# Performance work log

Hardware: AMD Instinct MI355X
Metric: run time of the kernel (lower is better)

The kernel has to match this reference:

```python
import jax, jax.numpy as jnp
import numpy as np

B, S, H, D = 4, 2048, 12, 64

def setup_inputs() -> dict:
    key = jax.random.key(0)
    kq, kk, kv_, kb = jax.random.split(key, 4)
    q = jax.random.normal(kq, (B, S, H, D), dtype=jnp.float32)
    k = jax.random.normal(kk, (B, S, H, D), dtype=jnp.float32)
    v = jax.random.normal(kv_, (B, S, H, D), dtype=jnp.float32)
    attn_bias = jax.random.normal(kb, (B, H, S, S), dtype=jnp.float32)
    return {"q": q, "k": k, "v": v, "attn_bias": attn_bias}

def reference(q, k, v, attn_bias):
    # flash_attn_func(q, k, v, attn_bias=bias): non-causal SDPA with additive bias,
    # softmax_scale = 1/sqrt(head_dim). Layout [b, s, h, d]; bias [b, h, sq, sk].
    scale = 1.0 / jnp.sqrt(jnp.asarray(q.shape[-1], q.dtype))
    # scores: [b, h, sq, sk]
    scores = jnp.einsum('bqhd,bkhd->bhqk', q, k) * scale + attn_bias
    probs = jax.nn.softmax(scores, axis=-1)
    out = jnp.einsum('bhqk,bkhd->bqhd', probs, v)
    return out
```

## Files before the change

kernel.cpp:

```cpp
#include <hip/hip_runtime.h>
#include <hip/hip_bf16.h>

#define B_ 4
#define S_ 2048
#define H_ 12
#define D_ 64
#define QT 64
#define KT 64
#define NQT (S_/QT)
#define NKT (S_/KT)
#define LOG2E 1.44269504088896340736f

typedef __bf16 bf16x8 __attribute__((ext_vector_type(8)));
typedef __bf16 bf16x4 __attribute__((ext_vector_type(4)));
typedef float  f32x4  __attribute__((ext_vector_type(4)));

__global__ __launch_bounds__(256, 2) void fa_fwd(
    const float* __restrict__ Q, const float* __restrict__ K,
    const float* __restrict__ V, const float* __restrict__ Bias,
    float* __restrict__ Out)
{
  __shared__ __attribute__((aligned(16))) __bf16 Qs[QT*72];
  __shared__ __attribute__((aligned(16))) __bf16 Ks[KT*72];
  __shared__ __attribute__((aligned(16))) __bf16 Vt[D_*68];
  __shared__ __attribute__((aligned(16))) __bf16 Ps[4*16*72];

  const int bid = blockIdx.x;
  const int qt  = bid & (NQT-1);
  const int bh  = bid >> 5;
  const int b   = bh / H_;
  const int h   = bh - b*H_;
  const int q0  = qt*QT;

  const int tid  = threadIdx.x;
  const int w    = tid >> 6;
  const int lane = tid & 63;
  const int g    = lane >> 4;
  const int c    = lane & 15;

  const float qscale = 0.125f * LOG2E;

  #pragma unroll
  for (int i = 0; i < 4; ++i) {
    int flat = i*256 + tid;
    int qr = flat >> 4;
    int d4 = (flat & 15) << 2;
    float4 qv = *(const float4*)(Q + (((size_t)b*S_ + q0 + qr)*H_ + h)*D_ + d4);
    bf16x4 pk;
    pk[0] = (__bf16)(qv.x * qscale); pk[1] = (__bf16)(qv.y * qscale);
    pk[2] = (__bf16)(qv.z * qscale); pk[3] = (__bf16)(qv.w * qscale);
    *(bf16x4*)&Qs[qr*72 + d4] = pk;
  }

  f32x4 Ov[4] = {};
  float m_i[4], l_i[4];
  #pragma unroll
  for (int r = 0; r < 4; ++r) { m_i[r] = -1e30f; l_i[r] = 0.f; }

  const size_t row_base = (size_t)q0 + 16*w + 4*g;
  const float* bb    = Bias + ((size_t)bh*S_ + row_base)*S_ + c;
  const float* kbase = K + ((size_t)b*S_*H_ + h)*D_;
  const float* vbase = V + ((size_t)b*S_*H_ + h)*D_;

  for (int kt = 0; kt < NKT; ++kt) {
    const int k0 = kt*KT;

    float bl[4][4];
    #pragma unroll
    for (int t = 0; t < 4; ++t)
      #pragma unroll
      for (int r = 0; r < 4; ++r)
        bl[t][r] = bb[(size_t)r*S_ + k0 + 16*t];

    __syncthreads();

    #pragma unroll
    for (int i = 0; i < 4; ++i) {
      int flat = i*256 + tid;
      int kr = flat >> 4;
      int d4 = (flat & 15) << 2;
      float4 kv = *(const float4*)(kbase + (size_t)(k0+kr)*H_*D_ + d4);
      bf16x4 pk;
      pk[0]=(__bf16)kv.x; pk[1]=(__bf16)kv.y; pk[2]=(__bf16)kv.z; pk[3]=(__bf16)kv.w;
      *(bf16x4*)&Ks[kr*72 + d4] = pk;
    }
    #pragma unroll
    for (int i = 0; i < 4; ++i) {
      int flat = i*256 + tid;
      int vr = flat >> 4;
      int d4 = (flat & 15) << 2;
      float4 vv = *(const float4*)(vbase + (size_t)(k0+vr)*H_*D_ + d4);
      Vt[(d4+0)*68 + vr] = (__bf16)vv.x;
      Vt[(d4+1)*68 + vr] = (__bf16)vv.y;
      Vt[(d4+2)*68 + vr] = (__bf16)vv.z;
      Vt[(d4+3)*68 + vr] = (__bf16)vv.w;
    }
    __syncthreads();

    bf16x8 aq0 = *(const bf16x8*)&Qs[(16*w + c)*72 + 8*g];
    bf16x8 aq1 = *(const bf16x8*)&Qs[(16*w + c)*72 + 32 + 8*g];
    float sc[4][4];
    #pragma unroll
    for (int t = 0; t < 4; ++t) {
      bf16x8 bk0 = *(const bf16x8*)&Ks[(16*t + c)*72 + 8*g];
      bf16x8 bk1 = *(const bf16x8*)&Ks[(16*t + c)*72 + 32 + 8*g];
      f32x4 acc = {};
      acc = __builtin_amdgcn_mfma_f32_16x16x32_bf16(aq0, bk0, acc, 0, 0, 0);
      acc = __builtin_amdgcn_mfma_f32_16x16x32_bf16(aq1, bk1, acc, 0, 0, 0);
      #pragma unroll
      for (int r = 0; r < 4; ++r)
        sc[t][r] = acc[r] + bl[t][r] * LOG2E;
    }

    #pragma unroll
    for (int r = 0; r < 4; ++r) {
      float mv = fmaxf(fmaxf(sc[0][r], sc[1][r]), fmaxf(sc[2][r], sc[3][r]));
      #pragma unroll
      for (int mask = 1; mask <= 8; mask <<= 1)
        mv = fmaxf(mv, __shfl_xor(mv, mask, 64));
      float mn = fmaxf(m_i[r], mv);
      float alpha = __builtin_amdgcn_exp2f(m_i[r] - mn);
      m_i[r] = mn;
      float rs = 0.f;
      #pragma unroll
      for (int t = 0; t < 4; ++t) {
        float p = __builtin_amdgcn_exp2f(sc[t][r] - mn);
        sc[t][r] = p;
        rs += p;
      }
      #pragma unroll
      for (int mask = 1; mask <= 8; mask <<= 1)
        rs += __shfl_xor(rs, mask, 64);
      l_i[r] = l_i[r]*alpha + rs;
      #pragma unroll
      for (int t = 0; t < 4; ++t)
        Ov[t][r] *= alpha;
    }

    #pragma unroll
    for (int t = 0; t < 4; ++t)
      #pragma unroll
      for (int r = 0; r < 4; ++r)
        Ps[w*1152 + (4*g + r)*72 + 16*t + c] = (__bf16)sc[t][r];

    #pragma unroll
    for (int hh = 0; hh < 2; ++hh) {
      bf16x8 ap = *(const bf16x8*)&Ps[w*1152 + c*72 + 32*hh + 8*g];
      #pragma unroll
      for (int t = 0; t < 4; ++t) {
        union { bf16x8 v8; bf16x4 v4[2]; } bv;
        bv.v4[0] = *(const bf16x4*)&Vt[(16*t + c)*68 + 32*hh + 8*g];
        bv.v4[1] = *(const bf16x4*)&Vt[(16*t + c)*68 + 32*hh + 8*g + 4];
        Ov[t] = __builtin_amdgcn_mfma_f32_16x16x32_bf16(ap, bv.v8, Ov[t], 0, 0, 0);
      }
    }
  }

  float* ob = Out + (((size_t)b*S_ + row_base)*H_ + h)*D_ + c;
  #pragma unroll
  for (int r = 0; r < 4; ++r) {
    float inv = 1.0f / l_i[r];
    #pragma unroll
    for (int t = 0; t < 4; ++t)
      ob[(size_t)r*H_*D_ + 16*t] = Ov[t][r] * inv;
  }
}

extern "C" void kernel_launch(void* const* d_in, const int* in_sizes, int n_in,
                              void* d_out, int out_size, void* d_ws, size_t ws_size,
                              hipStream_t stream) {
  const float* q    = (const float*)d_in[0];
  const float* k    = (const float*)d_in[1];
  const float* v    = (const float*)d_in[2];
  const float* bias = (const float*)d_in[3];
  float* out = (float*)d_out;
  dim3 grid(B_ * H_ * NQT);
  fa_fwd<<<grid, 256, 0, stream>>>(q, k, v, bias, out);
}
```

Before: 1.325 ms.

## Prefetch next K/V/bias tile into registers and remap blocks across XCDs

Loads for the next K, V and bias tiles are issued into registers during the current tile's compute, so global-memory latency overlaps with the MFMA and softmax work. Bias loads become nontemporal, and the bias is folded into the MFMA accumulator initialisation. Block IDs are remapped so that consecutive query tiles of one head land on the same XCD, which should improve L2 reuse of K/V. Launch bounds are raised to 4 blocks per SM, which limits registers even though the prefetch buffers add register pressure, so spills or lower occupancy are possible.

```diff
diff --git a/kernel.cpp b/kernel.cpp
--- a/kernel.cpp
+++ b/kernel.cpp
@@ -9,13 +9,14 @@
 #define KT 64
 #define NQT (S_/QT)
 #define NKT (S_/KT)
+#define NXCD 8
 #define LOG2E 1.44269504088896340736f
 
 typedef __bf16 bf16x8 __attribute__((ext_vector_type(8)));
 typedef __bf16 bf16x4 __attribute__((ext_vector_type(4)));
 typedef float  f32x4  __attribute__((ext_vector_type(4)));
 
-__global__ __launch_bounds__(256, 2) void fa_fwd(
+__global__ __launch_bounds__(256, 4) void fa_fwd(
     const float* __restrict__ Q, const float* __restrict__ K,
     const float* __restrict__ V, const float* __restrict__ Bias,
     float* __restrict__ Out)
@@ -25,7 +26,8 @@
   __shared__ __attribute__((aligned(16))) __bf16 Vt[D_*68];
   __shared__ __attribute__((aligned(16))) __bf16 Ps[4*16*72];
 
-  const int bid = blockIdx.x;
+  const int nper = (B_*H_*NQT)/NXCD;
+  const int bid  = (blockIdx.x % NXCD)*nper + (blockIdx.x / NXCD);
   const int qt  = bid & (NQT-1);
   const int bh  = bid >> 5;
   const int b   = bh / H_;
@@ -38,13 +40,14 @@
   const int g    = lane >> 4;
   const int c    = lane & 15;
 
+  const int sr0 = tid >> 4;
+  const int d4  = (tid & 15) << 2;
+
   const float qscale = 0.125f * LOG2E;
 
   #pragma unroll
   for (int i = 0; i < 4; ++i) {
-    int flat = i*256 + tid;
-    int qr = flat >> 4;
-    int d4 = (flat & 15) << 2;
+    const int qr = sr0 + 16*i;
     float4 qv = *(const float4*)(Q + (((size_t)b*S_ + q0 + qr)*H_ + h)*D_ + d4);
     bf16x4 pk;
     pk[0] = (__bf16)(qv.x * qscale); pk[1] = (__bf16)(qv.y * qscale);
@@ -59,43 +62,50 @@
 
   const size_t row_base = (size_t)q0 + 16*w + 4*g;
   const float* bb    = Bias + ((size_t)bh*S_ + row_base)*S_ + c;
-  const float* kbase = K + ((size_t)b*S_*H_ + h)*D_;
-  const float* vbase = V + ((size_t)b*S_*H_ + h)*D_;
+  const float* kbase = K + ((size_t)b*S_*H_ + h)*D_ + (size_t)sr0*H_*D_ + d4;
+  const float* vbase = V + ((size_t)b*S_*H_ + h)*D_ + (size_t)sr0*H_*D_ + d4;
+
+  float4 kreg[4], vreg[4];
+  #pragma unroll
+  for (int i = 0; i < 4; ++i) {
+    kreg[i] = *(const float4*)(kbase + (size_t)16*i*H_*D_);
+    vreg[i] = *(const float4*)(vbase + (size_t)16*i*H_*D_);
+  }
+  float bl[4][4];
+  #pragma unroll
+  for (int t = 0; t < 4; ++t)
+    #pragma unroll
+    for (int r = 0; r < 4; ++r)
+      bl[t][r] = __builtin_nontemporal_load(bb + (size_t)r*S_ + 16*t);
 
   for (int kt = 0; kt < NKT; ++kt) {
-    const int k0 = kt*KT;
-
-    float bl[4][4];
-    #pragma unroll
-    for (int t = 0; t < 4; ++t)
-      #pragma unroll
-      for (int r = 0; r < 4; ++r)
-        bl[t][r] = bb[(size_t)r*S_ + k0 + 16*t];
-
     __syncthreads();
 
     #pragma unroll
     for (int i = 0; i < 4; ++i) {
-      int flat = i*256 + tid;
-      int kr = flat >> 4;
-      int d4 = (flat & 15) << 2;
-      float4 kv = *(const float4*)(kbase + (size_t)(k0+kr)*H_*D_ + d4);
+      const int kr = sr0 + 16*i;
+      float4 kv = kreg[i];
       bf16x4 pk;
       pk[0]=(__bf16)kv.x; pk[1]=(__bf16)kv.y; pk[2]=(__bf16)kv.z; pk[3]=(__bf16)kv.w;
       *(bf16x4*)&Ks[kr*72 + d4] = pk;
-    }
-    #pragma unroll
-    for (int i = 0; i < 4; ++i) {
-      int flat = i*256 + tid;
-      int vr = flat >> 4;
-      int d4 = (flat & 15) << 2;
-      float4 vv = *(const float4*)(vbase + (size_t)(k0+vr)*H_*D_ + d4);
-      Vt[(d4+0)*68 + vr] = (__bf16)vv.x;
-      Vt[(d4+1)*68 + vr] = (__bf16)vv.y;
-      Vt[(d4+2)*68 + vr] = (__bf16)vv.z;
-      Vt[(d4+3)*68 + vr] = (__bf16)vv.w;
-    }
+      float4 vv = vreg[i];
+      Vt[(d4+0)*68 + kr] = (__bf16)vv.x;
+      Vt[(d4+1)*68 + kr] = (__bf16)vv.y;
+      Vt[(d4+2)*68 + kr] = (__bf16)vv.z;
+      Vt[(d4+3)*68 + kr] = (__bf16)vv.w;
+    }
+
     __syncthreads();
+
+    if (kt + 1 < NKT) {
+      const float* kp = kbase + (size_t)(kt+1)*KT*H_*D_;
+      const float* vp = vbase + (size_t)(kt+1)*KT*H_*D_;
+      #pragma unroll
+      for (int i = 0; i < 4; ++i) {
+        kreg[i] = *(const float4*)(kp + (size_t)16*i*H_*D_);
+        vreg[i] = *(const float4*)(vp + (size_t)16*i*H_*D_);
+      }
+    }
 
     bf16x8 aq0 = *(const bf16x8*)&Qs[(16*w + c)*72 + 8*g];
     bf16x8 aq1 = *(const bf16x8*)&Qs[(16*w + c)*72 + 32 + 8*g];
@@ -104,12 +114,23 @@
     for (int t = 0; t < 4; ++t) {
       bf16x8 bk0 = *(const bf16x8*)&Ks[(16*t + c)*72 + 8*g];
       bf16x8 bk1 = *(const bf16x8*)&Ks[(16*t + c)*72 + 32 + 8*g];
-      f32x4 acc = {};
+      f32x4 acc;
+      acc[0] = bl[t][0]*LOG2E; acc[1] = bl[t][1]*LOG2E;
+      acc[2] = bl[t][2]*LOG2E; acc[3] = bl[t][3]*LOG2E;
       acc = __builtin_amdgcn_mfma_f32_16x16x32_bf16(aq0, bk0, acc, 0, 0, 0);
       acc = __builtin_amdgcn_mfma_f32_16x16x32_bf16(aq1, bk1, acc, 0, 0, 0);
       #pragma unroll
       for (int r = 0; r < 4; ++r)
-        sc[t][r] = acc[r] + bl[t][r] * LOG2E;
+        sc[t][r] = acc[r];
+    }
+
+    if (kt + 1 < NKT) {
+      const float* bp = bb + (size_t)(kt+1)*KT;
+      #pragma unroll
+      for (int t = 0; t < 4; ++t)
+        #pragma unroll
+        for (int r = 0; r < 4; ++r)
+          bl[t][r] = __builtin_nontemporal_load(bp + (size_t)r*S_ + 16*t);
     }
 
     #pragma unroll
```

Measured after the change: 1.167 ms. 11.9% less time.
